# Optimization experiments

Measured on AMD Instinct MI355X. Metric: run time of the kernel, lower is better.

Reference implementation:

```python
import jax, jax.numpy as jnp
import numpy as np

D_MODEL = 768
HEADS = 12
D_K = D_MODEL // HEADS
NEG = -1e9


def setup_inputs() -> dict:
    key = jax.random.key(0)
    ks = jax.random.split(key, 12)
    B, S = 1, 4096
    q = jax.random.normal(ks[0], (B, S, D_MODEL), dtype=jnp.float32)
    k = jax.random.normal(ks[1], (B, S, D_MODEL), dtype=jnp.float32)
    v = jax.random.normal(ks[2], (B, S, D_MODEL), dtype=jnp.float32)
    mask = jax.random.randint(ks[3], (B, S, S), 0, 2, dtype=jnp.int32)
    sc = 1.0 / np.sqrt(D_MODEL)
    Wq = jax.random.normal(ks[4], (D_MODEL, D_MODEL), dtype=jnp.float32) * sc
    Wk = jax.random.normal(ks[5], (D_MODEL, D_MODEL), dtype=jnp.float32) * sc
    Wv = jax.random.normal(ks[6], (D_MODEL, D_MODEL), dtype=jnp.float32) * sc
    Wo = jax.random.normal(ks[7], (D_MODEL, D_MODEL), dtype=jnp.float32) * sc
    bq = jnp.zeros((D_MODEL,), jnp.float32)
    bk = jnp.zeros((D_MODEL,), jnp.float32)
    bv = jnp.zeros((D_MODEL,), jnp.float32)
    bo = jnp.zeros((D_MODEL,), jnp.float32)
    return {"q": q, "k": k, "v": v, "Wq": Wq, "bq": bq, "Wk": Wk, "bk": bk,
            "Wv": Wv, "bv": bv, "Wo": Wo, "bo": bo, "mask": mask}


def reference(q, k, v, Wq, bq, Wk, bk, Wv, bv, Wo, bo, mask) -> jnp.ndarray:
    B, S, _ = q.shape
    # projections (x @ W^T + b, matching nn.Linear)
    qh = (q @ Wq.T + bq).reshape(B, S, HEADS, D_K).transpose(0, 2, 1, 3)  # [B,h,S,dk]
    kh = (k @ Wk.T + bk).reshape(B, S, HEADS, D_K).transpose(0, 2, 1, 3)
    vh = (v @ Wv.T + bv).reshape(B, S, HEADS, D_K).transpose(0, 2, 1, 3)
    scores = jnp.einsum('bhqd,bhkd->bhqk', qh, kh) / jnp.sqrt(jnp.float32(D_K))
    scores = jnp.where(mask[:, None, :, :] == 0, jnp.float32(NEG), scores)
    attn = jax.nn.softmax(scores, axis=-1)  # dropout disabled (eval mode)
    ctx = jnp.einsum('bhqk,bhkd->bhqd', attn, vh)
    concat = ctx.transpose(0, 2, 1, 3).reshape(B, S, D_MODEL)
    return concat @ Wo.T + bo
```

## Files before the change

### kernel.cpp

```cpp
#include <hip/hip_runtime.h>

#define S_LEN 4096
#define DMODEL 768
#define NHEADS 12
#define DKH 64
#define SC2F 0.18033688011112042f

typedef __attribute__((ext_vector_type(8))) short bf16x8;
typedef __attribute__((ext_vector_type(4))) float f32x4;
typedef __attribute__((ext_vector_type(16))) float f32x16;
typedef __attribute__((ext_vector_type(4))) short s16x4;

#define AS1 __attribute__((address_space(1)))
#define AS3 __attribute__((address_space(3)))

__device__ __forceinline__ short f2bf(float f) {
    union { float f; unsigned u; } x; x.f = f;
    unsigned r = x.u + 0x7fffu + ((x.u >> 16) & 1u);
    return (short)(r >> 16);
}

__device__ __forceinline__ void gload_lds16(const void* g, void* l) {
    __builtin_amdgcn_global_load_lds((const AS1 void*)g, (AS3 void*)l, 16, 0, 0);
}

__global__ void cvt_bf16_3(const float* __restrict__ a, const float* __restrict__ b,
                           const float* __restrict__ c, short* __restrict__ da,
                           short* __restrict__ db, short* __restrict__ dc, int n8) {
    const float* s = blockIdx.z == 0 ? a : blockIdx.z == 1 ? b : c;
    short* d = blockIdx.z == 0 ? da : blockIdx.z == 1 ? db : dc;
    int stride = gridDim.x * blockDim.x;
    for (int i = blockIdx.x * blockDim.x + threadIdx.x; i < n8; i += stride) {
        float4 x = ((const float4*)s)[2 * i];
        float4 y = ((const float4*)s)[2 * i + 1];
        bf16x8 o;
        o[0] = f2bf(x.x); o[1] = f2bf(x.y); o[2] = f2bf(x.z); o[3] = f2bf(x.w);
        o[4] = f2bf(y.x); o[5] = f2bf(y.y); o[6] = f2bf(y.z); o[7] = f2bf(y.w);
        ((bf16x8*)d)[i] = o;
    }
}

__global__ void cvt_bf16_4(const float* __restrict__ a, const float* __restrict__ b,
                           const float* __restrict__ c, const float* __restrict__ e,
                           short* __restrict__ dst, int n8) {
    const float* s = blockIdx.z == 0 ? a : blockIdx.z == 1 ? b : blockIdx.z == 2 ? c : e;
    short* d = dst + (size_t)blockIdx.z * (size_t)n8 * 8;
    int stride = gridDim.x * blockDim.x;
    for (int i = blockIdx.x * blockDim.x + threadIdx.x; i < n8; i += stride) {
        float4 x = ((const float4*)s)[2 * i];
        float4 y = ((const float4*)s)[2 * i + 1];
        bf16x8 o;
        o[0] = f2bf(x.x); o[1] = f2bf(x.y); o[2] = f2bf(x.z); o[3] = f2bf(x.w);
        o[4] = f2bf(y.x); o[5] = f2bf(y.y); o[6] = f2bf(y.z); o[7] = f2bf(y.w);
        ((bf16x8*)d)[i] = o;
    }
}

__global__ void pack_mask_k(const int* __restrict__ mask, unsigned long long* __restrict__ mpT, int nwords) {
    int lane = threadIdx.x & 63;
    int wid = (blockIdx.x * blockDim.x + threadIdx.x) >> 6;
    int nw = (gridDim.x * blockDim.x) >> 6;
    for (int w = wid; w < nwords; w += nw) {
        int m = mask[(size_t)w * 64 + lane];
        unsigned long long b = __ballot(m != 0);
        if (lane == 0) mpT[(size_t)(w & 63) * S_LEN + (w >> 6)] = b;
    }
}

__global__ __launch_bounds__(256) void qkv_gemm(
    const short* __restrict__ qA, const short* __restrict__ kA, const short* __restrict__ vA,
    const short* __restrict__ Wqb, const short* __restrict__ Wkb, const short* __restrict__ Wvb,
    const float* __restrict__ bq, const float* __restrict__ bk, const float* __restrict__ bv,
    short* __restrict__ Qh, short* __restrict__ Kh, short* __restrict__ Vt)
{
    const int z = blockIdx.z;
    const short* A = z == 0 ? qA : z == 1 ? kA : vA;
    const short* B = z == 0 ? Wqb : z == 1 ? Wkb : Wvb;
    const float* bias = z == 0 ? bq : z == 1 ? bk : bv;

    __shared__ __align__(16) short As[128 * 64];
    __shared__ __align__(16) short Bs[128 * 64];
    const int tid = threadIdx.x;
    const int wv = tid >> 6, l = tid & 63;
    const int wr = wv >> 1, wc = wv & 1;
    const int g = l >> 4, hl = l & 15;
    const int m0 = blockIdx.x * 128, n0 = blockIdx.y * 128;
    const int Kd = DMODEL;

    f32x4 acc[4][4] = {};

    for (int kt = 0; kt < Kd; kt += 64) {
        __syncthreads();
        #pragma unroll
        for (int i = 0; i < 4; ++i) {
            int row = i * 32 + wv * 8 + (l >> 3);
            int csrc = (l & 7) ^ (row & 7);
            gload_lds16(A + (size_t)(m0 + row) * Kd + kt + csrc * 8, As + (i * 32 + wv * 8) * 64);
        }
        #pragma unroll
        for (int i = 0; i < 4; ++i) {
            int row = i * 32 + wv * 8 + (l >> 3);
            int csrc = (l & 7) ^ (row & 7);
            gload_lds16(B + (size_t)(n0 + row) * Kd + kt + csrc * 8, Bs + (i * 32 + wv * 8) * 64);
        }
        __syncthreads();
        #pragma unroll
        for (int s = 0; s < 2; ++s) {
            bf16x8 af[4], bf[4];
            #pragma unroll
            for (int m = 0; m < 4; ++m) {
                int row = wr * 64 + m * 16 + hl;
                int ch = (s * 4 + g) ^ (row & 7);
                af[m] = *(const bf16x8*)(As + row * 64 + ch * 8);
            }
            #pragma unroll
            for (int n = 0; n < 4; ++n) {
                int row = wc * 64 + n * 16 + hl;
                int ch = (s * 4 + g) ^ (row & 7);
                bf[n] = *(const bf16x8*)(Bs + row * 64 + ch * 8);
            }
            #pragma unroll
            for (int m = 0; m < 4; ++m)
                #pragma unroll
                for (int n = 0; n < 4; ++n)
                    acc[m][n] = __builtin_amdgcn_mfma_f32_16x16x32_bf16(af[m], bf[n], acc[m][n], 0, 0, 0);
        }
    }

    const float scale = (z == 0) ? SC2F : 1.0f;
    #pragma unroll
    for (int m = 0; m < 4; ++m) {
        #pragma unroll
        for (int n = 0; n < 4; ++n) {
            int gsb = m0 + wr * 64 + m * 16 + g * 4;
            int go = n0 + wc * 64 + n * 16 + hl;
            float bvv = bias[go];
            int hh = go >> 6, d = go & 63;
            if (z == 2) {
                s16x4 p;
                #pragma unroll
                for (int r = 0; r < 4; ++r) p[r] = f2bf(acc[m][n][r] + bvv);
                int gsb2 = (gsb & ~12) | ((gsb & 4) << 1) | ((gsb & 8) >> 1);
                *(s16x4*)(Vt + (size_t)hh * DKH * S_LEN + (size_t)d * S_LEN + gsb2) = p;
            } else {
                short* O = z ? Kh : Qh;
                #pragma unroll
                for (int r = 0; r < 4; ++r)
                    O[(size_t)hh * S_LEN * DKH + (size_t)(gsb + r) * DKH + d] = f2bf((acc[m][n][r] + bvv) * scale);
            }
        }
    }
}

__global__ __launch_bounds__(256) void gemm_out(
    const short* __restrict__ A, const short* __restrict__ B,
    const float* __restrict__ bias, float* __restrict__ O)
{
    __shared__ __align__(16) short As[128 * 64];
    __shared__ __align__(16) short Bs[128 * 64];
    const int tid = threadIdx.x;
    const int wv = tid >> 6, l = tid & 63;
    const int wr = wv >> 1, wc = wv & 1;
    const int g = l >> 4, hl = l & 15;
    const int m0 = blockIdx.x * 128, n0 = blockIdx.y * 128;
    const int Kd = DMODEL;

    f32x4 acc[4][4] = {};

    for (int kt = 0; kt < Kd; kt += 64) {
        __syncthreads();
        #pragma unroll
        for (int i = 0; i < 4; ++i) {
            int row = i * 32 + wv * 8 + (l >> 3);
            int csrc = (l & 7) ^ (row & 7);
            gload_lds16(A + (size_t)(m0 + row) * Kd + kt + csrc * 8, As + (i * 32 + wv * 8) * 64);
        }
        #pragma unroll
        for (int i = 0; i < 4; ++i) {
            int row = i * 32 + wv * 8 + (l >> 3);
            int csrc = (l & 7) ^ (row & 7);
            gload_lds16(B + (size_t)(n0 + row) * Kd + kt + csrc * 8, Bs + (i * 32 + wv * 8) * 64);
        }
        __syncthreads();
        #pragma unroll
        for (int s = 0; s < 2; ++s) {
            bf16x8 af[4], bf[4];
            #pragma unroll
            for (int m = 0; m < 4; ++m) {
                int row = wr * 64 + m * 16 + hl;
                int ch = (s * 4 + g) ^ (row & 7);
                af[m] = *(const bf16x8*)(As + row * 64 + ch * 8);
            }
            #pragma unroll
            for (int n = 0; n < 4; ++n) {
                int row = wc * 64 + n * 16 + hl;
                int ch = (s * 4 + g) ^ (row & 7);
                bf[n] = *(const bf16x8*)(Bs + row * 64 + ch * 8);
            }
            #pragma unroll
            for (int m = 0; m < 4; ++m)
                #pragma unroll
                for (int n = 0; n < 4; ++n)
                    acc[m][n] = __builtin_amdgcn_mfma_f32_16x16x32_bf16(af[m], bf[n], acc[m][n], 0, 0, 0);
        }
    }

    #pragma unroll
    for (int m = 0; m < 4; ++m) {
        #pragma unroll
        for (int n = 0; n < 4; ++n) {
            int gsb = m0 + wr * 64 + m * 16 + g * 4;
            int go = n0 + wc * 64 + n * 16 + hl;
            float bvv = bias[go];
            #pragma unroll
            for (int r = 0; r < 4; ++r)
                O[(size_t)(gsb + r) * DMODEL + go] = acc[m][n][r] + bvv;
        }
    }
}

__global__ __launch_bounds__(512) void flash_attn4(
    const short* __restrict__ Qh, const short* __restrict__ Kh,
    const short* __restrict__ Vt, const unsigned long long* __restrict__ mpT,
    short* __restrict__ ctx)
{
    __shared__ __align__(16) char pool[35328];

    const int tid = threadIdx.x;
    const int wv = tid >> 6, l = tid & 63;
    const int wq = wv >> 1, sp = wv & 1;
    const int hi = l >> 5, q = l & 31;

    int fid = blockIdx.x + (blockIdx.y << 5);
    int g = (fid & 7) * 48 + (fid >> 3);
    const int h = g >> 5;
    const int q0 = (g & 31) * 128;

    const short* Khb = Kh + (size_t)h * S_LEN * DKH;
    const short* Vtb = Vt + (size_t)h * DKH * S_LEN;
    const int qrow = q0 + wq * 32 + q;

    bf16x8 aq[4];
    #pragma unroll
    for (int s = 0; s < 4; ++s)
        aq[s] = *(const bf16x8*)(Qh + (size_t)h * S_LEN * DKH + (size_t)qrow * DKH + s * 16 + hi * 8);

    f32x16 acc[2] = {};
    float dacc[4] = {0.f, 0.f, 0.f, 0.f};

    short* Kl = (short*)(pool + sp * 8192);
    short* Vl = (short*)(pool + 16384 + sp * 8192);

    for (int i = 0; i < 32; ++i) {
        const int kt = i * 2 + sp;
        const int kv0 = kt * 64;
        __syncthreads();
        #pragma unroll
        for (int j = 0; j < 2; ++j) {
            int rp = (wq * 2 + j) * 4 + (l >> 4);
            int x = (l & 15) ^ (rp & 15);
            int row = rp * 2 + (x >> 3);
            int c = x & 7;
            gload_lds16(Khb + (size_t)(kv0 + row) * DKH + c * 8, Kl + (wq * 2 + j) * 512);
            gload_lds16(Vtb + (size_t)row * S_LEN + kv0 + c * 8, Vl + (wq * 2 + j) * 512);
        }
        unsigned long long w = mpT[(size_t)kt * S_LEN + qrow];
        __syncthreads();

        unsigned long long w2 = w >> (hi * 4);
        unsigned mlo = (unsigned)w2, mhi2 = (unsigned)(w2 >> 32);

        #pragma unroll
        for (int t = 0; t < 2; ++t) {
            const unsigned msk = t ? mhi2 : mlo;
            f32x16 st = {};
            __builtin_amdgcn_s_setprio(1);
            #pragma unroll
            for (int s = 0; s < 4; ++s) {
                int rowb = t * 32 + q;
                int rp = rowb >> 1;
                int ch = (((rowb & 1) << 3) + (s * 2 + hi)) ^ (rp & 15);
                bf16x8 kf = *(const bf16x8*)(Kl + rp * 128 + ch * 8);
                st = __builtin_amdgcn_mfma_f32_32x32x16_bf16(kf, aq[s], st, 0, 0, 0);
            }
            __builtin_amdgcn_s_setprio(0);
            float pf[16];
            #pragma unroll
            for (int r = 0; r < 16; ++r) {
                const int cbit = (r & 3) + 8 * (r >> 2);
                float sv = (msk & (1u << cbit)) ? st[r] : -120.0f;
                pf[r] = __builtin_amdgcn_exp2f(sv);
                dacc[r & 3] += pf[r];
            }
            __builtin_amdgcn_s_setprio(1);
            #pragma unroll
            for (int kk = 0; kk < 2; ++kk) {
                const float* pp = pf + kk * 8;
                union { unsigned u[4]; bf16x8 v; } pa;
                asm("v_cvt_pk_bf16_f32 %0, %1, %2" : "=v"(pa.u[0]) : "v"(pp[0]), "v"(pp[1]));
                asm("v_cvt_pk_bf16_f32 %0, %1, %2" : "=v"(pa.u[1]) : "v"(pp[2]), "v"(pp[3]));
                asm("v_cvt_pk_bf16_f32 %0, %1, %2" : "=v"(pa.u[2]) : "v"(pp[4]), "v"(pp[5]));
                asm("v_cvt_pk_bf16_f32 %0, %1, %2" : "=v"(pa.u[3]) : "v"(pp[6]), "v"(pp[7]));
                const int ks = t * 2 + kk;
                #pragma unroll
                for (int dt = 0; dt < 2; ++dt) {
                    int rowb = dt * 32 + q;
                    int rp = rowb >> 1;
                    int ch = (((rowb & 1) << 3) + (ks * 2 + hi)) ^ (rp & 15);
                    bf16x8 vf = *(const bf16x8*)(Vl + rp * 128 + ch * 8);
                    acc[dt] = __builtin_amdgcn_mfma_f32_32x32x16_bf16(pa.v, vf, acc[dt], 0, 0, 0);
                }
            }
            __builtin_amdgcn_s_setprio(0);
        }
    }

    const float dsum = dacc[0] + dacc[1] + dacc[2] + dacc[3];

    __syncthreads();
    float* accb = (float*)pool;
    float* ddb  = (float*)(pool + 32768);
    float* dinv = (float*)(pool + 34816);
    ddb[wv * 64 + l] = dsum;
    if (sp == 1) {
        #pragma unroll
        for (int dt = 0; dt < 2; ++dt)
            #pragma unroll
            for (int r = 0; r < 16; ++r)
                accb[(((wq * 2 + dt) * 16 + r) << 6) + l] = acc[dt][r];
    }
    __syncthreads();
    if (sp == 0) {
        float dq = ddb[(wq * 2) * 64 + q] + ddb[(wq * 2) * 64 + 32 + q]
                 + ddb[(wq * 2 + 1) * 64 + q] + ddb[(wq * 2 + 1) * 64 + 32 + q];
        if (hi == 0) dinv[wq * 32 + q] = 1.0f / dq;
    }
    __syncthreads();
    if (sp == 0) {
        #pragma unroll
        for (int dt = 0; dt < 2; ++dt) {
            #pragma unroll
            for (int r = 0; r < 16; ++r) {
                float o = acc[dt][r] + accb[(((wq * 2 + dt) * 16 + r) << 6) + l];
                int qo = (r & 3) + 8 * (r >> 2) + 4 * hi;
                float inv = dinv[wq * 32 + qo];
                ctx[(size_t)(q0 + wq * 32 + qo) * DMODEL + h * DKH + dt * 32 + q] = f2bf(o * inv);
            }
        }
    }
}

extern "C" void kernel_launch(void* const* d_in, const int* in_sizes, int n_in,
                              void* d_out, int out_size, void* d_ws, size_t ws_size,
                              hipStream_t stream) {
    (void)in_sizes; (void)n_in; (void)out_size; (void)ws_size;
    const float* q  = (const float*)d_in[0];
    const float* k  = (const float*)d_in[1];
    const float* v  = (const float*)d_in[2];
    const float* Wq = (const float*)d_in[3];
    const float* bq = (const float*)d_in[4];
    const float* Wk = (const float*)d_in[5];
    const float* bk = (const float*)d_in[6];
    const float* Wv = (const float*)d_in[7];
    const float* bv = (const float*)d_in[8];
    const float* Wo = (const float*)d_in[9];
    const float* bo = (const float*)d_in[10];
    const int* mask = (const int*)d_in[11];

    char* ws = (char*)d_ws;
    short* qb  = (short*)(ws + 0);
    short* kb  = (short*)(ws + 6291456);
    short* vb  = (short*)(ws + 12582912);
    short* Wqb = (short*)(ws + 18874368);
    short* Wkb = (short*)(ws + 20054016);
    short* Wvb = (short*)(ws + 21233664);
    short* Wob = (short*)(ws + 22413312);
    short* Qh  = (short*)(ws + 23592960);
    short* Kh  = (short*)(ws + 29884416);
    short* Vt  = (short*)(ws + 36175872);
    unsigned long long* mpT = (unsigned long long*)(ws + 42467328);
    short* ctx = (short*)(ws + 44564480);

    const int NQKV8 = S_LEN * DMODEL / 8;
    const int NW8 = DMODEL * DMODEL / 8;
    cvt_bf16_3<<<dim3(512, 1, 3), 256, 0, stream>>>(q, k, v, qb, kb, vb, NQKV8);
    cvt_bf16_4<<<dim3(288, 1, 4), 256, 0, stream>>>(Wq, Wk, Wv, Wo, Wqb, NW8);
    pack_mask_k<<<2048, 256, 0, stream>>>(mask, mpT, S_LEN * S_LEN / 64);

    qkv_gemm<<<dim3(S_LEN / 128, DMODEL / 128, 3), 256, 0, stream>>>(
        qb, kb, vb, Wqb, Wkb, Wvb, bq, bk, bv, Qh, Kh, Vt);

    flash_attn4<<<dim3(32, 12), 512, 0, stream>>>(Qh, Kh, Vt, mpT, ctx);

    gemm_out<<<dim3(S_LEN / 128, DMODEL / 128), 256, 0, stream>>>(ctx, Wob, bo, (float*)d_out);
}
```

Before: 164.8 us.

## Merge prep kernels into one launch and double KV tile per sync in attention

```diff
diff --git a/kernel.cpp b/kernel.cpp
--- a/kernel.cpp
+++ b/kernel.cpp
@@ -24,11 +24,37 @@
     __builtin_amdgcn_global_load_lds((const AS1 void*)g, (AS3 void*)l, 16, 0, 0);
 }
 
-__global__ void cvt_bf16_3(const float* __restrict__ a, const float* __restrict__ b,
-                           const float* __restrict__ c, short* __restrict__ da,
-                           short* __restrict__ db, short* __restrict__ dc, int n8) {
-    const float* s = blockIdx.z == 0 ? a : blockIdx.z == 1 ? b : c;
-    short* d = blockIdx.z == 0 ? da : blockIdx.z == 1 ? db : dc;
+__global__ void prep(const float* __restrict__ q, const float* __restrict__ k,
+                     const float* __restrict__ v, const float* __restrict__ Wq,
+                     const float* __restrict__ Wk, const float* __restrict__ Wv,
+                     const float* __restrict__ Wo,
+                     short* __restrict__ qb, short* __restrict__ kb,
+                     short* __restrict__ vb, short* __restrict__ Wb,
+                     const int* __restrict__ mask, unsigned long long* __restrict__ mpT) {
+    const int z = blockIdx.z;
+    if (z == 7) {
+        int lane = threadIdx.x & 63;
+        int wid = (blockIdx.x * blockDim.x + threadIdx.x) >> 6;
+        int nw = (gridDim.x * blockDim.x) >> 6;
+        for (int w = wid; w < S_LEN * S_LEN / 64; w += nw) {
+            int m = mask[(size_t)w * 64 + lane];
+            unsigned long long b = __ballot(m != 0);
+            if (lane == 0) mpT[(size_t)(w & 63) * S_LEN + (w >> 6)] = b;
+        }
+        return;
+    }
+    const float* s;
+    short* d;
+    int n8;
+    if (z < 3) {
+        s = z == 0 ? q : z == 1 ? k : v;
+        d = z == 0 ? qb : z == 1 ? kb : vb;
+        n8 = S_LEN * DMODEL / 8;
+    } else {
+        s = z == 3 ? Wq : z == 4 ? Wk : z == 5 ? Wv : Wo;
+        d = Wb + (size_t)(z - 3) * (DMODEL * DMODEL);
+        n8 = DMODEL * DMODEL / 8;
+    }
     int stride = gridDim.x * blockDim.x;
     for (int i = blockIdx.x * blockDim.x + threadIdx.x; i < n8; i += stride) {
         float4 x = ((const float4*)s)[2 * i];
@@ -37,33 +63,6 @@
         o[0] = f2bf(x.x); o[1] = f2bf(x.y); o[2] = f2bf(x.z); o[3] = f2bf(x.w);
         o[4] = f2bf(y.x); o[5] = f2bf(y.y); o[6] = f2bf(y.z); o[7] = f2bf(y.w);
         ((bf16x8*)d)[i] = o;
-    }
-}
-
-__global__ void cvt_bf16_4(const float* __restrict__ a, const float* __restrict__ b,
-                           const float* __restrict__ c, const float* __restrict__ e,
-                           short* __restrict__ dst, int n8) {
-    const float* s = blockIdx.z == 0 ? a : blockIdx.z == 1 ? b : blockIdx.z == 2 ? c : e;
-    short* d = dst + (size_t)blockIdx.z * (size_t)n8 * 8;
-    int stride = gridDim.x * blockDim.x;
-    for (int i = blockIdx.x * blockDim.x + threadIdx.x; i < n8; i += stride) {
-        float4 x = ((const float4*)s)[2 * i];
-        float4 y = ((const float4*)s)[2 * i + 1];
-        bf16x8 o;
-        o[0] = f2bf(x.x); o[1] = f2bf(x.y); o[2] = f2bf(x.z); o[3] = f2bf(x.w);
-        o[4] = f2bf(y.x); o[5] = f2bf(y.y); o[6] = f2bf(y.z); o[7] = f2bf(y.w);
-        ((bf16x8*)d)[i] = o;
-    }
-}
-
-__global__ void pack_mask_k(const int* __restrict__ mask, unsigned long long* __restrict__ mpT, int nwords) {
-    int lane = threadIdx.x & 63;
-    int wid = (blockIdx.x * blockDim.x + threadIdx.x) >> 6;
-    int nw = (gridDim.x * blockDim.x) >> 6;
-    for (int w = wid; w < nwords; w += nw) {
-        int m = mask[(size_t)w * 64 + lane];
-        unsigned long long b = __ballot(m != 0);
-        if (lane == 0) mpT[(size_t)(w & 63) * S_LEN + (w >> 6)] = b;
     }
 }
 
@@ -219,12 +218,12 @@
     }
 }
 
-__global__ __launch_bounds__(512) void flash_attn4(
+__global__ __launch_bounds__(512) void flash_attn5(
     const short* __restrict__ Qh, const short* __restrict__ Kh,
     const short* __restrict__ Vt, const unsigned long long* __restrict__ mpT,
     short* __restrict__ ctx)
 {
-    __shared__ __align__(16) char pool[35328];
+    __shared__ __align__(16) char pool[65536];
 
     const int tid = threadIdx.x;
     const int wv = tid >> 6, l = tid & 63;
@@ -248,70 +247,83 @@
     f32x16 acc[2] = {};
     float dacc[4] = {0.f, 0.f, 0.f, 0.f};
 
-    short* Kl = (short*)(pool + sp * 8192);
-    short* Vl = (short*)(pool + 16384 + sp * 8192);
-
-    for (int i = 0; i < 32; ++i) {
-        const int kt = i * 2 + sp;
-        const int kv0 = kt * 64;
-        __syncthreads();
-        #pragma unroll
-        for (int j = 0; j < 2; ++j) {
-            int rp = (wq * 2 + j) * 4 + (l >> 4);
-            int x = (l & 15) ^ (rp & 15);
-            int row = rp * 2 + (x >> 3);
-            int c = x & 7;
-            gload_lds16(Khb + (size_t)(kv0 + row) * DKH + c * 8, Kl + (wq * 2 + j) * 512);
-            gload_lds16(Vtb + (size_t)row * S_LEN + kv0 + c * 8, Vl + (wq * 2 + j) * 512);
-        }
-        unsigned long long w = mpT[(size_t)kt * S_LEN + qrow];
-        __syncthreads();
-
-        unsigned long long w2 = w >> (hi * 4);
-        unsigned mlo = (unsigned)w2, mhi2 = (unsigned)(w2 >> 32);
-
-        #pragma unroll
-        for (int t = 0; t < 2; ++t) {
-            const unsigned msk = t ? mhi2 : mlo;
-            f32x16 st = {};
-            __builtin_amdgcn_s_setprio(1);
-            #pragma unroll
-            for (int s = 0; s < 4; ++s) {
-                int rowb = t * 32 + q;
-                int rp = rowb >> 1;
-                int ch = (((rowb & 1) << 3) + (s * 2 + hi)) ^ (rp & 15);
-                bf16x8 kf = *(const bf16x8*)(Kl + rp * 128 + ch * 8);
-                st = __builtin_amdgcn_mfma_f32_32x32x16_bf16(kf, aq[s], st, 0, 0, 0);
-            }
-            __builtin_amdgcn_s_setprio(0);
-            float pf[16];
-            #pragma unroll
-            for (int r = 0; r < 16; ++r) {
-                const int cbit = (r & 3) + 8 * (r >> 2);
-                float sv = (msk & (1u << cbit)) ? st[r] : -120.0f;
-                pf[r] = __builtin_amdgcn_exp2f(sv);
-                dacc[r & 3] += pf[r];
-            }
-            __builtin_amdgcn_s_setprio(1);
-            #pragma unroll
-            for (int kk = 0; kk < 2; ++kk) {
-                const float* pp = pf + kk * 8;
-                union { unsigned u[4]; bf16x8 v; } pa;
-                asm("v_cvt_pk_bf16_f32 %0, %1, %2" : "=v"(pa.u[0]) : "v"(pp[0]), "v"(pp[1]));
-                asm("v_cvt_pk_bf16_f32 %0, %1, %2" : "=v"(pa.u[1]) : "v"(pp[2]), "v"(pp[3]));
-                asm("v_cvt_pk_bf16_f32 %0, %1, %2" : "=v"(pa.u[2]) : "v"(pp[4]), "v"(pp[5]));
-                asm("v_cvt_pk_bf16_f32 %0, %1, %2" : "=v"(pa.u[3]) : "v"(pp[6]), "v"(pp[7]));
-                const int ks = t * 2 + kk;
-                #pragma unroll
-                for (int dt = 0; dt < 2; ++dt) {
-                    int rowb = dt * 32 + q;
+    short* const poolS = (short*)pool;
+
+    for (int i = 0; i < 16; ++i) {
+        __syncthreads();
+        #pragma unroll
+        for (int j = 0; j < 8; ++j) {
+            const int u = wv * 8 + j;
+            const int isV = u >> 5;
+            const int u5 = u & 31;
+            const int spt = u5 >> 4;
+            const int sub = (u5 >> 3) & 1;
+            const int iu = u5 & 7;
+            const int rp = iu * 4 + (l >> 4);
+            const int x = (l & 15) ^ (rp & 15);
+            const int row = rp * 2 + (x >> 3);
+            const int c = x & 7;
+            const int kvb = i * 256 + spt * 128 + sub * 64;
+            short* dst = poolS + isV * 16384 + spt * 8192 + sub * 4096 + iu * 512;
+            if (isV == 0)
+                gload_lds16(Khb + (size_t)(kvb + row) * DKH + c * 8, dst);
+            else
+                gload_lds16(Vtb + (size_t)row * S_LEN + kvb + c * 8, dst);
+        }
+        unsigned long long w0 = mpT[(size_t)(i * 4 + sp * 2) * S_LEN + qrow];
+        unsigned long long w1 = mpT[(size_t)(i * 4 + sp * 2 + 1) * S_LEN + qrow];
+        __syncthreads();
+
+        #pragma unroll
+        for (int wi = 0; wi < 2; ++wi) {
+            const short* Ksub = poolS + sp * 8192 + wi * 4096;
+            const short* Vsub = poolS + 16384 + sp * 8192 + wi * 4096;
+            unsigned long long w2 = (wi ? w1 : w0) >> (hi * 4);
+            unsigned mlo = (unsigned)w2, mhi2 = (unsigned)(w2 >> 32);
+
+            #pragma unroll
+            for (int t = 0; t < 2; ++t) {
+                const unsigned msk = t ? mhi2 : mlo;
+                f32x16 st = {};
+                __builtin_amdgcn_s_setprio(1);
+                #pragma unroll
+                for (int s = 0; s < 4; ++s) {
+                    int rowb = t * 32 + q;
                     int rp = rowb >> 1;
-                    int ch = (((rowb & 1) << 3) + (ks * 2 + hi)) ^ (rp & 15);
-                    bf16x8 vf = *(const bf16x8*)(Vl + rp * 128 + ch * 8);
-                    acc[dt] = __builtin_amdgcn_mfma_f32_32x32x16_bf16(pa.v, vf, acc[dt], 0, 0, 0);
+                    int ch = (((rowb & 1) << 3) + (s * 2 + hi)) ^ (rp & 15);
+                    bf16x8 kf = *(const bf16x8*)(Ksub + rp * 128 + ch * 8);
+                    st = __builtin_amdgcn_mfma_f32_32x32x16_bf16(kf, aq[s], st, 0, 0, 0);
                 }
-            }
-            __builtin_amdgcn_s_setprio(0);
+                __builtin_amdgcn_s_setprio(0);
+                float pf[16];
+                #pragma unroll
+                for (int r = 0; r < 16; ++r) {
+                    const int cbit = (r & 3) + 8 * (r >> 2);
+                    float sv = (msk & (1u << cbit)) ? st[r] : -120.0f;
+                    pf[r] = __builtin_amdgcn_exp2f(sv);
+                    dacc[r & 3] += pf[r];
+                }
+                __builtin_amdgcn_s_setprio(1);
+                #pragma unroll
+                for (int kk = 0; kk < 2; ++kk) {
+                    const float* pp = pf + kk * 8;
+                    union { unsigned u[4]; bf16x8 v; } pa;
+                    asm("v_cvt_pk_bf16_f32 %0, %1, %2" : "=v"(pa.u[0]) : "v"(pp[0]), "v"(pp[1]));
+                    asm("v_cvt_pk_bf16_f32 %0, %1, %2" : "=v"(pa.u[1]) : "v"(pp[2]), "v"(pp[3]));
+                    asm("v_cvt_pk_bf16_f32 %0, %1, %2" : "=v"(pa.u[2]) : "v"(pp[4]), "v"(pp[5]));
+                    asm("v_cvt_pk_bf16_f32 %0, %1, %2" : "=v"(pa.u[3]) : "v"(pp[6]), "v"(pp[7]));
+                    const int ks = t * 2 + kk;
+                    #pragma unroll
+                    for (int dt = 0; dt < 2; ++dt) {
+                        int rowb = dt * 32 + q;
+                        int rp = rowb >> 1;
+                        int ch = (((rowb & 1) << 3) + (ks * 2 + hi)) ^ (rp & 15);
+                        bf16x8 vf = *(const bf16x8*)(Vsub + rp * 128 + ch * 8);
+                        acc[dt] = __builtin_amdgcn_mfma_f32_32x32x16_bf16(pa.v, vf, acc[dt], 0, 0, 0);
+                    }
+                }
+                __builtin_amdgcn_s_setprio(0);
+            }
         }
     }
 
@@ -381,16 +393,12 @@
     unsigned long long* mpT = (unsigned long long*)(ws + 42467328);
     short* ctx = (short*)(ws + 44564480);
 
-    const int NQKV8 = S_LEN * DMODEL / 8;
-    const int NW8 = DMODEL * DMODEL / 8;
-    cvt_bf16_3<<<dim3(512, 1, 3), 256, 0, stream>>>(q, k, v, qb, kb, vb, NQKV8);
-    cvt_bf16_4<<<dim3(288, 1, 4), 256, 0, stream>>>(Wq, Wk, Wv, Wo, Wqb, NW8);
-    pack_mask_k<<<2048, 256, 0, stream>>>(mask, mpT, S_LEN * S_LEN / 64);
+    prep<<<dim3(512, 1, 8), 256, 0, stream>>>(q, k, v, Wq, Wk, Wv, Wo, qb, kb, vb, Wqb, mask, mpT);
 
     qkv_gemm<<<dim3(S_LEN / 128, DMODEL / 128, 3), 256, 0, stream>>>(
         qb, kb, vb, Wqb, Wkb, Wvb, bq, bk, bv, Qh, Kh, Vt);
 
-    flash_attn4<<<dim3(32, 12), 512, 0, stream>>>(Qh, Kh, Vt, mpT, ctx);
+    flash_attn5<<<dim3(32, 12), 512, 0, stream>>>(Qh, Kh, Vt, mpT, ctx);
 
     gemm_out<<<dim3(S_LEN / 128, DMODEL / 128), 256, 0, stream>>>(ctx, Wob, bo, (float*)d_out);
 }
```

Result: slower. 219.5 us (+33.2%).

## Split attention over key halves and merge partial results in a separate kernel

Applied to the files above, without the earlier changes.

```diff
diff --git a/kernel.cpp b/kernel.cpp
--- a/kernel.cpp
+++ b/kernel.cpp
@@ -18,6 +18,12 @@
     union { float f; unsigned u; } x; x.f = f;
     unsigned r = x.u + 0x7fffu + ((x.u >> 16) & 1u);
     return (short)(r >> 16);
+}
+
+__device__ __forceinline__ float bf2f(short s) {
+    union { unsigned u; float f; } x;
+    x.u = ((unsigned)(unsigned short)s) << 16;
+    return x.f;
 }
 
 __device__ __forceinline__ void gload_lds16(const void* g, void* l) {
@@ -219,10 +225,10 @@
     }
 }
 
-__global__ __launch_bounds__(512) void flash_attn4(
+__global__ __launch_bounds__(512, 6) void flash_attn6(
     const short* __restrict__ Qh, const short* __restrict__ Kh,
     const short* __restrict__ Vt, const unsigned long long* __restrict__ mpT,
-    short* __restrict__ ctx)
+    short* __restrict__ po, float* __restrict__ pd)
 {
     __shared__ __align__(16) char pool[35328];
 
@@ -231,10 +237,12 @@
     const int wq = wv >> 1, sp = wv & 1;
     const int hi = l >> 5, q = l & 31;
 
-    int fid = blockIdx.x + (blockIdx.y << 5);
-    int g = (fid & 7) * 48 + (fid >> 3);
-    const int h = g >> 5;
-    const int q0 = (g & 31) * 128;
+    int fid = blockIdx.x;
+    int g = (fid & 7) * 96 + (fid >> 3);
+    const int h = g >> 6;
+    const int sub = g & 63;
+    const int half = sub >> 5;
+    const int q0 = (sub & 31) * 128;
 
     const short* Khb = Kh + (size_t)h * S_LEN * DKH;
     const short* Vtb = Vt + (size_t)h * DKH * S_LEN;
@@ -251,8 +259,8 @@
     short* Kl = (short*)(pool + sp * 8192);
     short* Vl = (short*)(pool + 16384 + sp * 8192);
 
-    for (int i = 0; i < 32; ++i) {
-        const int kt = i * 2 + sp;
+    for (int i = 0; i < 16; ++i) {
+        const int kt = half * 32 + i * 2 + sp;
         const int kv0 = kt * 64;
         __syncthreads();
         #pragma unroll
@@ -320,7 +328,6 @@
     __syncthreads();
     float* accb = (float*)pool;
     float* ddb  = (float*)(pool + 32768);
-    float* dinv = (float*)(pool + 34816);
     ddb[wv * 64 + l] = dsum;
     if (sp == 1) {
         #pragma unroll
@@ -333,21 +340,34 @@
     if (sp == 0) {
         float dq = ddb[(wq * 2) * 64 + q] + ddb[(wq * 2) * 64 + 32 + q]
                  + ddb[(wq * 2 + 1) * 64 + q] + ddb[(wq * 2 + 1) * 64 + 32 + q];
-        if (hi == 0) dinv[wq * 32 + q] = 1.0f / dq;
-    }
-    __syncthreads();
-    if (sp == 0) {
+        if (hi == 0) pd[(size_t)half * (NHEADS * S_LEN) + (size_t)h * S_LEN + q0 + wq * 32 + q] = dq;
         #pragma unroll
         for (int dt = 0; dt < 2; ++dt) {
             #pragma unroll
             for (int r = 0; r < 16; ++r) {
                 float o = acc[dt][r] + accb[(((wq * 2 + dt) * 16 + r) << 6) + l];
                 int qo = (r & 3) + 8 * (r >> 2) + 4 * hi;
-                float inv = dinv[wq * 32 + qo];
-                ctx[(size_t)(q0 + wq * 32 + qo) * DMODEL + h * DKH + dt * 32 + q] = f2bf(o * inv);
-            }
-        }
-    }
+                po[((size_t)(half * NHEADS + h) * S_LEN + q0 + wq * 32 + qo) * DKH + dt * 32 + q] = f2bf(o);
+            }
+        }
+    }
+}
+
+__global__ __launch_bounds__(256) void flash_merge(const short* __restrict__ po,
+                                                   const float* __restrict__ pd,
+                                                   short* __restrict__ ctx)
+{
+    const int i = blockIdx.x * 256 + threadIdx.x;
+    const int hq = i >> 3;
+    const int h = hq >> 12, qrow = hq & 4095;
+    bf16x8 a = ((const bf16x8*)po)[i];
+    bf16x8 b = ((const bf16x8*)po)[i + NHEADS * S_LEN * DKH / 8];
+    float inv = 1.0f / (pd[hq] + pd[NHEADS * S_LEN + hq]);
+    bf16x8 o;
+    #pragma unroll
+    for (int e = 0; e < 8; ++e)
+        o[e] = f2bf((bf2f(a[e]) + bf2f(b[e])) * inv);
+    *(bf16x8*)(ctx + (size_t)qrow * DMODEL + h * DKH + (i & 7) * 8) = o;
 }
 
 extern "C" void kernel_launch(void* const* d_in, const int* in_sizes, int n_in,
@@ -380,6 +400,8 @@
     short* Vt  = (short*)(ws + 36175872);
     unsigned long long* mpT = (unsigned long long*)(ws + 42467328);
     short* ctx = (short*)(ws + 44564480);
+    short* po = (short*)(ws + 0);
+    float* pd = (float*)(ws + 12582912);
 
     const int NQKV8 = S_LEN * DMODEL / 8;
     const int NW8 = DMODEL * DMODEL / 8;
@@ -390,7 +412,8 @@
     qkv_gemm<<<dim3(S_LEN / 128, DMODEL / 128, 3), 256, 0, stream>>>(
         qb, kb, vb, Wqb, Wkb, Wvb, bq, bk, bv, Qh, Kh, Vt);
 
-    flash_attn4<<<dim3(32, 12), 512, 0, stream>>>(Qh, Kh, Vt, mpT, ctx);
+    flash_attn6<<<768, 512, 0, stream>>>(Qh, Kh, Vt, mpT, po, pd);
+    flash_merge<<<1536, 256, 0, stream>>>(po, pd, ctx);
 
     gemm_out<<<dim3(S_LEN / 128, DMODEL / 128), 256, 0, stream>>>(ctx, Wob, bo, (float*)d_out);
 }
```

Measured after the change: 316.2 us. 1.92x slower.
